# Optimization experiments

Measured on AMD Instinct MI355X. Metric: run time of the kernel, lower is better.

Reference implementation:

```python
import jax, jax.numpy as jnp
import numpy as np

B, T, D, H = 4, 2048, 512, 8
DK = D // H

def setup_inputs() -> dict:
    key = jax.random.key(0)
    ks = jax.random.split(key, 5)
    s = 1.0 / np.sqrt(D)
    return {
        "x": jax.random.normal(ks[0], (B, T, D), dtype=jnp.float32),
        "Wq": jax.random.normal(ks[1], (D, D), dtype=jnp.float32) * s,
        "bq": jnp.zeros((D,), dtype=jnp.float32),
        "Wk": jax.random.normal(ks[2], (D, D), dtype=jnp.float32) * s,
        "bk": jnp.zeros((D,), dtype=jnp.float32),
        "Wv": jax.random.normal(ks[3], (D, D), dtype=jnp.float32) * s,
        "bv": jnp.zeros((D,), dtype=jnp.float32),
        "Wo": jax.random.normal(ks[4], (D, D), dtype=jnp.float32) * s,
        "bo": jnp.zeros((D,), dtype=jnp.float32),
    }

def reference(x, Wq, bq, Wk, bk, Wv, bv, Wo, bo):
    # Linear projections (torch Linear: x @ W.T + b); split into heads.
    q = (x @ Wq.T + bq).reshape(B, T, H, DK)  # [B,T,H,dk]
    k = (x @ Wk.T + bk).reshape(B, T, H, DK)
    v = (x @ Wv.T + bv).reshape(B, T, H, DK)
    scale = 1.0 / np.sqrt(DK)
    # scores: [B,H,T,T]
    scores = jnp.einsum("bqhd,bkhd->bhqk", q, k) * scale
    attn = jax.nn.softmax(scores, axis=-1)
    ctx = jnp.einsum("bhqk,bkhd->bqhd", attn, v).reshape(B, T, D)
    return ctx @ Wo.T + bo
```

## Files before the change

### kernel.cpp

```cpp
#include <hip/hip_runtime.h>
#include <stdint.h>

#define NB 4
#define NT 2048
#define ND 512
#define NH 8
#define NDK 64
#define NM (NB*NT)

typedef __attribute__((ext_vector_type(8))) short short8;
typedef __attribute__((ext_vector_type(4))) short bs4;
typedef __attribute__((ext_vector_type(4))) float f32x4;

__device__ __forceinline__ unsigned short f2b(float f) {
    union { float f; uint32_t u; } v; v.f = f;
    return (unsigned short)((v.u + 0x7FFFu + ((v.u >> 16) & 1u)) >> 16);
}

__device__ __forceinline__ void load_lds16(const void* g, void* l) {
    void* gn = const_cast<void*>(g);
    __builtin_amdgcn_global_load_lds((__attribute__((address_space(1))) void*)gn,
                                     (__attribute__((address_space(3))) void*)l,
                                     16, 0, 0);
}

__global__ void convert_all(const float* __restrict__ x,  const float* __restrict__ wq,
                            const float* __restrict__ wk, const float* __restrict__ wv,
                            const float* __restrict__ wo, unsigned short* __restrict__ dst) {
    size_t i = ((size_t)blockIdx.x * 256 + threadIdx.x) * 4;
    const float* src; size_t off;
    if (i < 4194304) { src = x; off = i; }
    else {
        size_t j = i - 4194304;
        src = (j < 262144) ? wq : (j < 524288) ? wk : (j < 786432) ? wv : wo;
        off = j & 262143;
    }
    f32x4 v = *(const f32x4*)(src + off);
    ushort4 r;
    r.x = f2b(v[0]); r.y = f2b(v[1]); r.z = f2b(v[2]); r.w = f2b(v[3]);
    *(ushort4*)(dst + i) = r;
}

__global__ __launch_bounds__(256, 3) void proj_gemm(
        const unsigned short* __restrict__ X,
        const unsigned short* __restrict__ Wbase,
        const float* __restrict__ bias0, const float* __restrict__ bias1,
        const float* __restrict__ bias2,
        unsigned short* __restrict__ Obase, unsigned short* __restrict__ VTb,
        float scale0) {
    const int z = blockIdx.z;
    const float* bias = (z == 0) ? bias0 : (z == 1 ? bias1 : bias2);
    const float scale = (z == 0) ? scale0 : 1.0f;

    int rowBase, colBase;
    const unsigned short *Ap, *Bp;
    if (z == 2) {
        rowBase = blockIdx.x * 128;  colBase = blockIdx.y * 128;
        Ap = Wbase + 2 * (ND * ND);  Bp = X;
    } else {
        rowBase = blockIdx.y * 128;  colBase = blockIdx.x * 128;
        Ap = X;                      Bp = Wbase + (size_t)z * (ND * ND);
    }

    __shared__ alignas(16) unsigned short ldsA[128 * 32];
    __shared__ alignas(16) unsigned short ldsW[128 * 32];

    const int tid = threadIdx.x;
    const int lane = tid & 63, wave = tid >> 6;
    const int quad = lane >> 4, l15 = lane & 15;
    const int wm = wave >> 1, wn = wave & 1;

    const int rS = wave * 16 + (lane >> 2);
    const int kS = (lane & 3) * 8;
    const unsigned short* gA = Ap + (size_t)(rowBase + rS) * ND + kS;
    const unsigned short* gW = Bp + (size_t)(colBase + rS) * ND + kS;
    unsigned short* lA = ldsA + wave * 512;
    unsigned short* lW = ldsW + wave * 512;

    f32x4 acc[4][4];
#pragma unroll
    for (int i = 0; i < 4; i++)
#pragma unroll
        for (int j = 0; j < 4; j++) acc[i][j] = (f32x4)0.0f;

    for (int kt = 0; kt < ND / 32; ++kt) {
        __syncthreads();
        load_lds16(gA,            lA);
        load_lds16(gA + 64 * ND,  lA + 2048);
        load_lds16(gW,            lW);
        load_lds16(gW + 64 * ND,  lW + 2048);
        gA += 32; gW += 32;
        __syncthreads();

        short8 af[4], bfm[4];
#pragma unroll
        for (int mt = 0; mt < 4; ++mt)
            af[mt] = *(const short8*)(ldsA + (wm * 64 + mt * 16 + l15) * 32 + quad * 8);
#pragma unroll
        for (int nt = 0; nt < 4; ++nt)
            bfm[nt] = *(const short8*)(ldsW + (wn * 64 + nt * 16 + l15) * 32 + quad * 8);
#pragma unroll
        for (int mt = 0; mt < 4; ++mt)
#pragma unroll
            for (int nt = 0; nt < 4; ++nt)
                acc[mt][nt] = __builtin_amdgcn_mfma_f32_16x16x32_bf16(
                    af[mt], bfm[nt], acc[mt][nt], 0, 0, 0);
    }

    if (z == 2) {
        const int bz = colBase >> 11;
        const int t0 = colBase & 2047;
        unsigned short* VTo = VTb + ((size_t)(bz * 512 + rowBase)) * NT + t0;
#pragma unroll
        for (int mt = 0; mt < 4; mt++)
#pragma unroll
            for (int reg = 0; reg < 4; reg++) {
                int m = wm * 64 + mt * 16 + quad * 4 + reg;
                float bm = bias[rowBase + m];
                unsigned short* dst = VTo + (size_t)m * NT + wn * 64 + l15;
#pragma unroll
                for (int nt = 0; nt < 4; nt++)
                    dst[nt * 16] = f2b(acc[mt][nt][reg] + bm);
            }
    } else {
        float biasr[4];
#pragma unroll
        for (int nt = 0; nt < 4; nt++)
            biasr[nt] = bias[colBase + wn * 64 + nt * 16 + l15];
        unsigned short* Oz = Obase + (size_t)z * ((size_t)NM * ND);
#pragma unroll
        for (int mt = 0; mt < 4; mt++) {
            int row = rowBase + wm * 64 + mt * 16 + quad * 4;
#pragma unroll
            for (int reg = 0; reg < 4; reg++) {
                unsigned short* dst = Oz + (size_t)(row + reg) * ND + colBase + wn * 64 + l15;
#pragma unroll
                for (int nt = 0; nt < 4; nt++)
                    dst[nt * 16] = f2b((acc[mt][nt][reg] + biasr[nt]) * scale);
            }
        }
    }
}

__global__ __launch_bounds__(256, 4) void out_gemm(
        const unsigned short* __restrict__ A, const unsigned short* __restrict__ W,
        const float* __restrict__ bias, float* __restrict__ OF) {
    __shared__ alignas(16) unsigned short ldsA[64 * 32];
    __shared__ alignas(16) unsigned short ldsW[128 * 32];

    const int tid = threadIdx.x;
    const int lane = tid & 63, wave = tid >> 6;
    const int quad = lane >> 4, l15 = lane & 15;
    const int wm = wave >> 1, wn = wave & 1;
    const int rowBase = blockIdx.y * 64;
    const int colBase = blockIdx.x * 128;

    const int rW = wave * 16 + (lane >> 2);
    const int kS = (lane & 3) * 8;
    const unsigned short* gA = A + (size_t)(rowBase + rW) * ND + kS;
    const unsigned short* gW = W + (size_t)(colBase + rW) * ND + kS;
    unsigned short* lA = ldsA + wave * 512;
    unsigned short* lW = ldsW + wave * 512;

    f32x4 acc[2][4];
#pragma unroll
    for (int mt = 0; mt < 2; mt++)
#pragma unroll
        for (int nt = 0; nt < 4; nt++) acc[mt][nt] = (f32x4)0.0f;

    for (int kt = 0; kt < ND / 32; ++kt) {
        __syncthreads();
        load_lds16(gA,           lA);
        load_lds16(gW,           lW);
        load_lds16(gW + 64 * ND, lW + 2048);
        gA += 32; gW += 32;
        __syncthreads();

        short8 af[2], bfm[4];
#pragma unroll
        for (int mt = 0; mt < 2; ++mt)
            af[mt] = *(const short8*)(ldsA + (wm * 32 + mt * 16 + l15) * 32 + quad * 8);
#pragma unroll
        for (int nt = 0; nt < 4; ++nt)
            bfm[nt] = *(const short8*)(ldsW + (wn * 64 + nt * 16 + l15) * 32 + quad * 8);
#pragma unroll
        for (int mt = 0; mt < 2; ++mt)
#pragma unroll
            for (int nt = 0; nt < 4; ++nt)
                acc[mt][nt] = __builtin_amdgcn_mfma_f32_16x16x32_bf16(
                    af[mt], bfm[nt], acc[mt][nt], 0, 0, 0);
    }

    float biasr[4];
#pragma unroll
    for (int nt = 0; nt < 4; nt++)
        biasr[nt] = bias[colBase + wn * 64 + nt * 16 + l15];

#pragma unroll
    for (int mt = 0; mt < 2; mt++)
#pragma unroll
        for (int reg = 0; reg < 4; reg++) {
            int row = rowBase + wm * 32 + mt * 16 + quad * 4 + reg;
            float* dst = OF + (size_t)row * ND + colBase + wn * 64 + l15;
#pragma unroll
            for (int nt = 0; nt < 4; nt++)
                dst[nt * 16] = acc[mt][nt][reg] + biasr[nt];
        }
}

__global__ __launch_bounds__(256, 4) void attn_kernel(
        const unsigned short* __restrict__ Qb, const unsigned short* __restrict__ Kb,
        const unsigned short* __restrict__ VTb, unsigned short* __restrict__ Cb) {
    const int qt = blockIdx.x, h = blockIdx.y, b = blockIdx.z;
    __shared__ alignas(16) unsigned short Ks[64 * 64];
    __shared__ alignas(16) unsigned short Vt[64 * 64];

    const int tid = threadIdx.x, lane = tid & 63, wave = tid >> 6;
    const int quad = lane >> 4, l15 = lane & 15;
    const size_t headOff = (size_t)h * NDK;
    const size_t rowB = (size_t)b * NT;
    const unsigned short* VT = VTb + (size_t)(b * NH + h) * ((size_t)NDK * NT);

    short8 aq[2];
#pragma unroll
    for (int ks = 0; ks < 2; ++ks)
        aq[ks] = *(const short8*)(Qb + (rowB + qt * 64 + wave * 16 + l15) * ND
                                  + headOff + ks * 32 + quad * 8);

    const int r0 = wave * 16 + (lane >> 3);
    const int g0 = (lane & 7) ^ (r0 & 7);
    const unsigned short* Kbh = Kb + rowB * ND + headOff;
    const unsigned short* gK0 = Kbh + (size_t)r0 * ND + g0 * 8;
    const unsigned short* gK1 = Kbh + (size_t)(r0 + 8) * ND + g0 * 8;
    const unsigned short* gV0 = VT + (size_t)r0 * NT + g0 * 8;
    const unsigned short* gV1 = VT + (size_t)(r0 + 8) * NT + g0 * 8;
    unsigned short* ldsK = Ks + wave * 1024;
    unsigned short* ldsV = Vt + wave * 1024;

    const int swz = l15 & 7;
    const int qh = quad >> 1, qlo = quad & 1;
    const unsigned short* kb0 = Ks + l15 * 64 + ((quad ^ swz) * 8);
    const unsigned short* kb1 = Ks + l15 * 64 + (((4 + quad) ^ swz) * 8);
    const unsigned short* vbp[4];
#pragma unroll
    for (int kt = 0; kt < 4; ++kt)
        vbp[kt] = Vt + l15 * 64 + (((kt * 2 + qh) ^ swz) * 8) + qlo * 4;

    f32x4 o[4];
#pragma unroll
    for (int nt = 0; nt < 4; nt++) o[nt] = (f32x4)0.0f;
    float lacc = 0.0f;

    for (int kv = 0; kv < NT / 64; ++kv) {
        __syncthreads();
        load_lds16(gK0, ldsK);
        load_lds16(gK1, ldsK + 512);
        load_lds16(gV0, ldsV);
        load_lds16(gV1, ldsV + 512);
        gK0 += 64 * ND; gK1 += 64 * ND; gV0 += 64; gV1 += 64;
        __syncthreads();

        bs4 pk[4];
#pragma unroll
        for (int kt = 0; kt < 4; ++kt) {
            f32x4 st = (f32x4)0.0f;
            st = __builtin_amdgcn_mfma_f32_16x16x32_bf16(
                *(const short8*)(kb0 + kt * 1024), aq[0], st, 0, 0, 0);
            st = __builtin_amdgcn_mfma_f32_16x16x32_bf16(
                *(const short8*)(kb1 + kt * 1024), aq[1], st, 0, 0, 0);
            float p0 = exp2f(st[0]), p1 = exp2f(st[1]);
            float p2 = exp2f(st[2]), p3 = exp2f(st[3]);
            lacc += (p0 + p1) + (p2 + p3);
            uint32_t lo = __builtin_amdgcn_perm(__float_as_uint(p1), __float_as_uint(p0),
                                                0x07060302u);
            uint32_t hi = __builtin_amdgcn_perm(__float_as_uint(p3), __float_as_uint(p2),
                                                0x07060302u);
            union { uint32_t w[2]; bs4 v; } cvt;
            cvt.w[0] = lo; cvt.w[1] = hi;
            pk[kt] = cvt.v;
        }

#pragma unroll
        for (int kt = 0; kt < 4; ++kt)
#pragma unroll
            for (int nt = 0; nt < 4; ++nt)
                o[nt] = __builtin_amdgcn_mfma_f32_16x16x16bf16_1k(
                    pk[kt], *(const bs4*)(vbp[kt] + nt * 1024), o[nt], 0, 0, 0);
    }

    lacc += __shfl_xor(lacc, 16);
    lacc += __shfl_xor(lacc, 32);

#pragma unroll
    for (int reg = 0; reg < 4; ++reg) {
        float inv = 1.0f / __shfl(lacc, quad * 4 + reg);
        size_t row = rowB + qt * 64 + wave * 16 + quad * 4 + reg;
#pragma unroll
        for (int nt = 0; nt < 4; ++nt)
            Cb[row * ND + headOff + nt * 16 + l15] = f2b(o[nt][reg] * inv);
    }
}

extern "C" void kernel_launch(void* const* d_in, const int* in_sizes, int n_in,
                              void* d_out, int out_size, void* d_ws, size_t ws_size,
                              hipStream_t stream) {
    (void)in_sizes; (void)n_in; (void)out_size; (void)ws_size;
    const float* x  = (const float*)d_in[0];
    const float* Wq = (const float*)d_in[1];
    const float* bq = (const float*)d_in[2];
    const float* Wk = (const float*)d_in[3];
    const float* bk = (const float*)d_in[4];
    const float* Wv = (const float*)d_in[5];
    const float* bv = (const float*)d_in[6];
    const float* Wo = (const float*)d_in[7];
    const float* bo = (const float*)d_in[8];
    float* out = (float*)d_out;

    unsigned short* ws  = (unsigned short*)d_ws;
    unsigned short* xb  = ws;
    unsigned short* wqb = xb + 4194304;
    unsigned short* Qb  = wqb + 4 * 262144;
    unsigned short* Kb  = Qb + 4194304;
    unsigned short* VTb = Kb + 4194304;
    unsigned short* Cb  = VTb + 4194304;
    unsigned short* wob = wqb + 3 * 262144;

    convert_all<<<5120, 256, 0, stream>>>(x, Wq, Wk, Wv, Wo, ws);

    const float qscale = 0.125f * 1.44269504f;
    proj_gemm<<<dim3(4, 64, 3), 256, 0, stream>>>(xb, wqb, bq, bk, bv, Qb, VTb, qscale);
    attn_kernel<<<dim3(32, 8, 4), 256, 0, stream>>>(Qb, Kb, VTb, Cb);
    out_gemm<<<dim3(4, 128), 256, 0, stream>>>(Cb, wob, bo, out);
}
```

Measured before the change: 179.2 us.

## Deepen GEMM K-tiles with swizzled LDS and give attention waves two row tiles

```diff
diff --git a/kernel.cpp b/kernel.cpp
--- a/kernel.cpp
+++ b/kernel.cpp
@@ -62,20 +62,21 @@
         Ap = X;                      Bp = Wbase + (size_t)z * (ND * ND);
     }
 
-    __shared__ alignas(16) unsigned short ldsA[128 * 32];
-    __shared__ alignas(16) unsigned short ldsW[128 * 32];
+    __shared__ alignas(16) unsigned short ldsA[128 * 64];
+    __shared__ alignas(16) unsigned short ldsW[128 * 64];
 
     const int tid = threadIdx.x;
     const int lane = tid & 63, wave = tid >> 6;
     const int quad = lane >> 4, l15 = lane & 15;
     const int wm = wave >> 1, wn = wave & 1;
 
-    const int rS = wave * 16 + (lane >> 2);
-    const int kS = (lane & 3) * 8;
-    const unsigned short* gA = Ap + (size_t)(rowBase + rS) * ND + kS;
-    const unsigned short* gW = Bp + (size_t)(colBase + rS) * ND + kS;
-    unsigned short* lA = ldsA + wave * 512;
-    unsigned short* lW = ldsW + wave * 512;
+    const int rS = tid >> 3;
+    const int gc = (tid & 7) ^ (rS & 7);
+    const unsigned short* gA = Ap + (size_t)(rowBase + rS) * ND + gc * 8;
+    const unsigned short* gW = Bp + (size_t)(colBase + rS) * ND + gc * 8;
+    const int ldst = wave * 512;
+
+    const int swz = l15 & 7;
 
     f32x4 acc[4][4];
 #pragma unroll
@@ -83,28 +84,34 @@
 #pragma unroll
         for (int j = 0; j < 4; j++) acc[i][j] = (f32x4)0.0f;
 
-    for (int kt = 0; kt < ND / 32; ++kt) {
-        __syncthreads();
-        load_lds16(gA,            lA);
-        load_lds16(gA + 64 * ND,  lA + 2048);
-        load_lds16(gW,            lW);
-        load_lds16(gW + 64 * ND,  lW + 2048);
-        gA += 32; gW += 32;
-        __syncthreads();
-
-        short8 af[4], bfm[4];
-#pragma unroll
-        for (int mt = 0; mt < 4; ++mt)
-            af[mt] = *(const short8*)(ldsA + (wm * 64 + mt * 16 + l15) * 32 + quad * 8);
-#pragma unroll
-        for (int nt = 0; nt < 4; ++nt)
-            bfm[nt] = *(const short8*)(ldsW + (wn * 64 + nt * 16 + l15) * 32 + quad * 8);
-#pragma unroll
-        for (int mt = 0; mt < 4; ++mt)
+    for (int kt = 0; kt < ND / 64; ++kt) {
+        __syncthreads();
+#pragma unroll
+        for (int c = 0; c < 4; ++c) {
+            load_lds16(gA + (size_t)c * 32 * ND, ldsA + c * 2048 + ldst);
+            load_lds16(gW + (size_t)c * 32 * ND, ldsW + c * 2048 + ldst);
+        }
+        gA += 64; gW += 64;
+        __syncthreads();
+
+#pragma unroll
+        for (int ks = 0; ks < 2; ++ks) {
+            short8 af[4], bfm[4];
+#pragma unroll
+            for (int mt = 0; mt < 4; ++mt)
+                af[mt] = *(const short8*)(ldsA + (wm * 64 + mt * 16 + l15) * 64
+                                          + (((ks * 4 + quad) ^ swz) * 8));
 #pragma unroll
             for (int nt = 0; nt < 4; ++nt)
-                acc[mt][nt] = __builtin_amdgcn_mfma_f32_16x16x32_bf16(
-                    af[mt], bfm[nt], acc[mt][nt], 0, 0, 0);
+                bfm[nt] = *(const short8*)(ldsW + (wn * 64 + nt * 16 + l15) * 64
+                                           + (((ks * 4 + quad) ^ swz) * 8));
+#pragma unroll
+            for (int mt = 0; mt < 4; ++mt)
+#pragma unroll
+                for (int nt = 0; nt < 4; ++nt)
+                    acc[mt][nt] = __builtin_amdgcn_mfma_f32_16x16x32_bf16(
+                        af[mt], bfm[nt], acc[mt][nt], 0, 0, 0);
+        }
     }
 
     if (z == 2) {
@@ -145,8 +152,8 @@
 __global__ __launch_bounds__(256, 4) void out_gemm(
         const unsigned short* __restrict__ A, const unsigned short* __restrict__ W,
         const float* __restrict__ bias, float* __restrict__ OF) {
-    __shared__ alignas(16) unsigned short ldsA[64 * 32];
-    __shared__ alignas(16) unsigned short ldsW[128 * 32];
+    __shared__ alignas(16) unsigned short ldsA[64 * 64];
+    __shared__ alignas(16) unsigned short ldsW[128 * 64];
 
     const int tid = threadIdx.x;
     const int lane = tid & 63, wave = tid >> 6;
@@ -155,12 +162,12 @@
     const int rowBase = blockIdx.y * 64;
     const int colBase = blockIdx.x * 128;
 
-    const int rW = wave * 16 + (lane >> 2);
-    const int kS = (lane & 3) * 8;
-    const unsigned short* gA = A + (size_t)(rowBase + rW) * ND + kS;
-    const unsigned short* gW = W + (size_t)(colBase + rW) * ND + kS;
-    unsigned short* lA = ldsA + wave * 512;
-    unsigned short* lW = ldsW + wave * 512;
+    const int rS = tid >> 3;
+    const int gc = (tid & 7) ^ (rS & 7);
+    const unsigned short* gA = A + (size_t)(rowBase + rS) * ND + gc * 8;
+    const unsigned short* gW = W + (size_t)(colBase + rS) * ND + gc * 8;
+    const int ldst = wave * 512;
+    const int swz = l15 & 7;
 
     f32x4 acc[2][4];
 #pragma unroll
@@ -168,27 +175,35 @@
 #pragma unroll
         for (int nt = 0; nt < 4; nt++) acc[mt][nt] = (f32x4)0.0f;
 
-    for (int kt = 0; kt < ND / 32; ++kt) {
-        __syncthreads();
-        load_lds16(gA,           lA);
-        load_lds16(gW,           lW);
-        load_lds16(gW + 64 * ND, lW + 2048);
-        gA += 32; gW += 32;
-        __syncthreads();
-
-        short8 af[2], bfm[4];
-#pragma unroll
-        for (int mt = 0; mt < 2; ++mt)
-            af[mt] = *(const short8*)(ldsA + (wm * 32 + mt * 16 + l15) * 32 + quad * 8);
-#pragma unroll
-        for (int nt = 0; nt < 4; ++nt)
-            bfm[nt] = *(const short8*)(ldsW + (wn * 64 + nt * 16 + l15) * 32 + quad * 8);
-#pragma unroll
-        for (int mt = 0; mt < 2; ++mt)
+    for (int kt = 0; kt < ND / 64; ++kt) {
+        __syncthreads();
+#pragma unroll
+        for (int c = 0; c < 2; ++c)
+            load_lds16(gA + (size_t)c * 32 * ND, ldsA + c * 2048 + ldst);
+#pragma unroll
+        for (int c = 0; c < 4; ++c)
+            load_lds16(gW + (size_t)c * 32 * ND, ldsW + c * 2048 + ldst);
+        gA += 64; gW += 64;
+        __syncthreads();
+
+#pragma unroll
+        for (int ks = 0; ks < 2; ++ks) {
+            short8 af[2], bfm[4];
+#pragma unroll
+            for (int mt = 0; mt < 2; ++mt)
+                af[mt] = *(const short8*)(ldsA + (wm * 32 + mt * 16 + l15) * 64
+                                          + (((ks * 4 + quad) ^ swz) * 8));
 #pragma unroll
             for (int nt = 0; nt < 4; ++nt)
-                acc[mt][nt] = __builtin_amdgcn_mfma_f32_16x16x32_bf16(
-                    af[mt], bfm[nt], acc[mt][nt], 0, 0, 0);
+                bfm[nt] = *(const short8*)(ldsW + (wn * 64 + nt * 16 + l15) * 64
+                                           + (((ks * 4 + quad) ^ swz) * 8));
+#pragma unroll
+            for (int mt = 0; mt < 2; ++mt)
+#pragma unroll
+                for (int nt = 0; nt < 4; ++nt)
+                    acc[mt][nt] = __builtin_amdgcn_mfma_f32_16x16x32_bf16(
+                        af[mt], bfm[nt], acc[mt][nt], 0, 0, 0);
+        }
     }
 
     float biasr[4];
@@ -208,7 +223,7 @@
         }
 }
 
-__global__ __launch_bounds__(256, 4) void attn_kernel(
+__global__ __launch_bounds__(128, 2) void attn_kernel(
         const unsigned short* __restrict__ Qb, const unsigned short* __restrict__ Kb,
         const unsigned short* __restrict__ VTb, unsigned short* __restrict__ Cb) {
     const int qt = blockIdx.x, h = blockIdx.y, b = blockIdx.z;
@@ -221,21 +236,19 @@
     const size_t rowB = (size_t)b * NT;
     const unsigned short* VT = VTb + (size_t)(b * NH + h) * ((size_t)NDK * NT);
 
-    short8 aq[2];
-#pragma unroll
-    for (int ks = 0; ks < 2; ++ks)
-        aq[ks] = *(const short8*)(Qb + (rowB + qt * 64 + wave * 16 + l15) * ND
-                                  + headOff + ks * 32 + quad * 8);
-
-    const int r0 = wave * 16 + (lane >> 3);
-    const int g0 = (lane & 7) ^ (r0 & 7);
-    const unsigned short* Kbh = Kb + rowB * ND + headOff;
-    const unsigned short* gK0 = Kbh + (size_t)r0 * ND + g0 * 8;
-    const unsigned short* gK1 = Kbh + (size_t)(r0 + 8) * ND + g0 * 8;
-    const unsigned short* gV0 = VT + (size_t)r0 * NT + g0 * 8;
-    const unsigned short* gV1 = VT + (size_t)(r0 + 8) * NT + g0 * 8;
-    unsigned short* ldsK = Ks + wave * 1024;
-    unsigned short* ldsV = Vt + wave * 1024;
+    short8 aq[2][2];
+#pragma unroll
+    for (int mt = 0; mt < 2; ++mt)
+#pragma unroll
+        for (int ks = 0; ks < 2; ++ks)
+            aq[mt][ks] = *(const short8*)(Qb + (rowB + qt * 64 + wave * 32 + mt * 16 + l15) * ND
+                                          + headOff + ks * 32 + quad * 8);
+
+    const int rS = tid >> 3;
+    const int gcs = (tid & 7) ^ (rS & 7);
+    const unsigned short* gK = Kb + rowB * ND + headOff + (size_t)rS * ND + gcs * 8;
+    const unsigned short* gV = VT + (size_t)rS * NT + gcs * 8;
+    const int ldst = wave * 512;
 
     const int swz = l15 & 7;
     const int qh = quad >> 1, qlo = quad & 1;
@@ -246,58 +259,69 @@
     for (int kt = 0; kt < 4; ++kt)
         vbp[kt] = Vt + l15 * 64 + (((kt * 2 + qh) ^ swz) * 8) + qlo * 4;
 
-    f32x4 o[4];
-#pragma unroll
-    for (int nt = 0; nt < 4; nt++) o[nt] = (f32x4)0.0f;
-    float lacc = 0.0f;
+    f32x4 o[2][4];
+#pragma unroll
+    for (int mt = 0; mt < 2; mt++)
+#pragma unroll
+        for (int nt = 0; nt < 4; nt++) o[mt][nt] = (f32x4)0.0f;
+    float lacc[2] = {0.f, 0.f};
 
     for (int kv = 0; kv < NT / 64; ++kv) {
         __syncthreads();
-        load_lds16(gK0, ldsK);
-        load_lds16(gK1, ldsK + 512);
-        load_lds16(gV0, ldsV);
-        load_lds16(gV1, ldsV + 512);
-        gK0 += 64 * ND; gK1 += 64 * ND; gV0 += 64; gV1 += 64;
-        __syncthreads();
-
-        bs4 pk[4];
+#pragma unroll
+        for (int c = 0; c < 4; ++c) {
+            load_lds16(gK + (size_t)c * 16 * ND, Ks + c * 1024 + ldst);
+            load_lds16(gV + (size_t)c * 16 * NT, Vt + c * 1024 + ldst);
+        }
+        gK += 64 * ND; gV += 64;
+        __syncthreads();
+
+        bs4 pk[4][2];
 #pragma unroll
         for (int kt = 0; kt < 4; ++kt) {
-            f32x4 st = (f32x4)0.0f;
-            st = __builtin_amdgcn_mfma_f32_16x16x32_bf16(
-                *(const short8*)(kb0 + kt * 1024), aq[0], st, 0, 0, 0);
-            st = __builtin_amdgcn_mfma_f32_16x16x32_bf16(
-                *(const short8*)(kb1 + kt * 1024), aq[1], st, 0, 0, 0);
-            float p0 = exp2f(st[0]), p1 = exp2f(st[1]);
-            float p2 = exp2f(st[2]), p3 = exp2f(st[3]);
-            lacc += (p0 + p1) + (p2 + p3);
-            uint32_t lo = __builtin_amdgcn_perm(__float_as_uint(p1), __float_as_uint(p0),
-                                                0x07060302u);
-            uint32_t hi = __builtin_amdgcn_perm(__float_as_uint(p3), __float_as_uint(p2),
-                                                0x07060302u);
-            union { uint32_t w[2]; bs4 v; } cvt;
-            cvt.w[0] = lo; cvt.w[1] = hi;
-            pk[kt] = cvt.v;
+            short8 ak0 = *(const short8*)(kb0 + kt * 1024);
+            short8 ak1 = *(const short8*)(kb1 + kt * 1024);
+#pragma unroll
+            for (int mt = 0; mt < 2; ++mt) {
+                f32x4 st = (f32x4)0.0f;
+                st = __builtin_amdgcn_mfma_f32_16x16x32_bf16(ak0, aq[mt][0], st, 0, 0, 0);
+                st = __builtin_amdgcn_mfma_f32_16x16x32_bf16(ak1, aq[mt][1], st, 0, 0, 0);
+                float p0 = exp2f(st[0]), p1 = exp2f(st[1]);
+                float p2 = exp2f(st[2]), p3 = exp2f(st[3]);
+                lacc[mt] += (p0 + p1) + (p2 + p3);
+                uint32_t lo = __builtin_amdgcn_perm(__float_as_uint(p1), __float_as_uint(p0),
+                                                    0x07060302u);
+                uint32_t hi = __builtin_amdgcn_perm(__float_as_uint(p3), __float_as_uint(p2),
+                                                    0x07060302u);
+                union { uint32_t w[2]; bs4 v; } cvt;
+                cvt.w[0] = lo; cvt.w[1] = hi;
+                pk[kt][mt] = cvt.v;
+            }
         }
 
 #pragma unroll
         for (int kt = 0; kt < 4; ++kt)
 #pragma unroll
+            for (int nt = 0; nt < 4; ++nt) {
+                bs4 vbf = *(const bs4*)(vbp[kt] + nt * 1024);
+                o[0][nt] = __builtin_amdgcn_mfma_f32_16x16x16bf16_1k(pk[kt][0], vbf, o[0][nt], 0, 0, 0);
+                o[1][nt] = __builtin_amdgcn_mfma_f32_16x16x16bf16_1k(pk[kt][1], vbf, o[1][nt], 0, 0, 0);
+            }
+    }
+
+#pragma unroll
+    for (int mt = 0; mt < 2; ++mt) {
+        float l = lacc[mt];
+        l += __shfl_xor(l, 16);
+        l += __shfl_xor(l, 32);
+#pragma unroll
+        for (int reg = 0; reg < 4; ++reg) {
+            float inv = 1.0f / __shfl(l, quad * 4 + reg);
+            size_t row = rowB + qt * 64 + wave * 32 + mt * 16 + quad * 4 + reg;
+#pragma unroll
             for (int nt = 0; nt < 4; ++nt)
-                o[nt] = __builtin_amdgcn_mfma_f32_16x16x16bf16_1k(
-                    pk[kt], *(const bs4*)(vbp[kt] + nt * 1024), o[nt], 0, 0, 0);
-    }
-
-    lacc += __shfl_xor(lacc, 16);
-    lacc += __shfl_xor(lacc, 32);
-
-#pragma unroll
-    for (int reg = 0; reg < 4; ++reg) {
-        float inv = 1.0f / __shfl(lacc, quad * 4 + reg);
-        size_t row = rowB + qt * 64 + wave * 16 + quad * 4 + reg;
-#pragma unroll
-        for (int nt = 0; nt < 4; ++nt)
-            Cb[row * ND + headOff + nt * 16 + l15] = f2b(o[nt][reg] * inv);
+                Cb[row * ND + headOff + nt * 16 + l15] = f2b(o[mt][nt][reg] * inv);
+        }
     }
 }
 
@@ -329,6 +353,6 @@
 
     const float qscale = 0.125f * 1.44269504f;
     proj_gemm<<<dim3(4, 64, 3), 256, 0, stream>>>(xb, wqb, bq, bk, bv, Qb, VTb, qscale);
-    attn_kernel<<<dim3(32, 8, 4), 256, 0, stream>>>(Qb, Kb, VTb, Cb);
+    attn_kernel<<<dim3(32, 8, 4), 128, 0, stream>>>(Qb, Kb, VTb, Cb);
     out_gemm<<<dim3(4, 128), 256, 0, stream>>>(Cb, wob, bo, out);
 }
```

New measurement: 188.8 us. +5.3%, slower.
